# Optimization experiments

Measured on AMD Instinct MI355X. Metric: run time of the kernel, lower is better.

Reference implementation:

```python
import jax, jax.numpy as jnp
import numpy as np

B, N, D, NH, NP, H, W = 4, 4096, 256, 8, 8, 256, 256
HD = D // NH  # head_dims = 32


def _mlp(x, w1, b1, w2, b2):
    return jax.nn.relu(x @ w1 + b1) @ w2 + b2


def _grid_sample(value, grid):
    """Bilinear grid_sample, align_corners=False, zero padding.
    value: [M, C, Hh, Ww]; grid: [M, n, p, 2] with (x, y) in [-1, 1].
    Returns [M, C, n, p] (matches torch F.grid_sample output layout)."""
    M, C, Hh, Ww = value.shape
    x = (grid[..., 0] + 1.0) * (Ww * 0.5) - 0.5
    y = (grid[..., 1] + 1.0) * (Hh * 0.5) - 0.5
    x0 = jnp.floor(x)
    y0 = jnp.floor(y)
    wx1 = x - x0
    wy1 = y - y0
    vflat = value.reshape(M, C, Hh * Ww)

    def gather(yy, xx):
        valid = (xx >= 0) & (xx <= Ww - 1) & (yy >= 0) & (yy <= Hh - 1)
        idx = (jnp.clip(yy, 0, Hh - 1) * Ww + jnp.clip(xx, 0, Ww - 1)).astype(jnp.int32)
        g = jnp.take_along_axis(vflat, idx.reshape(M, 1, -1), axis=2)
        return g.reshape(M, C, idx.shape[1], idx.shape[2]) * valid[:, None].astype(value.dtype)

    return (gather(y0, x0) * ((1.0 - wy1) * (1.0 - wx1))[:, None]
            + gather(y0, x0 + 1.0) * ((1.0 - wy1) * wx1)[:, None]
            + gather(y0 + 1.0, x0) * (wy1 * (1.0 - wx1))[:, None]
            + gather(y0 + 1.0, x0 + 1.0) * (wy1 * wx1)[:, None])


def setup_inputs() -> dict:
    key = jax.random.key(0)
    ks = jax.random.split(key, 10)
    s = 0.02
    f32 = jnp.float32
    return {
        "ba_query": jax.random.normal(ks[0], (B, N, D), f32),
        "ref_pos": jax.random.uniform(ks[1], (B, N, 2), f32, minval=-0.9, maxval=0.9),
        "bev_feat": jax.random.normal(ks[2], (B, D, H, W), f32),
        "so_w1": jax.random.normal(ks[3], (D, D), f32) * s,
        "so_b1": jnp.zeros((D,), f32),
        "so_w2": jax.random.normal(ks[4], (D, NH * NP * 2), f32) * s,
        "so_b2": jnp.zeros((NH * NP * 2,), f32),
        "aw_w1": jax.random.normal(ks[5], (D, D), f32) * s,
        "aw_b1": jnp.zeros((D,), f32),
        "aw_w2": jax.random.normal(ks[6], (D, NH * NP), f32) * s,
        "aw_b2": jnp.zeros((NH * NP,), f32),
        "vp_w": jax.random.normal(ks[7], (HD, HD), f32) * s,  # 1x1 conv == per-pixel linear
        "vp_b": jnp.zeros((HD,), f32),
        "op_w1": jax.random.normal(ks[8], (D, D), f32) * s,
        "op_b1": jnp.zeros((D,), f32),
        "op_w2": jax.random.normal(ks[9], (D, D), f32) * s,
        "op_b2": jnp.zeros((D,), f32),
    }


def reference(ba_query, ref_pos, bev_feat,
              so_w1, so_b1, so_w2, so_b2,
              aw_w1, aw_b1, aw_w2, aw_b2,
              vp_w, vp_b,
              op_w1, op_b1, op_w2, op_b2):
    Bb, Dd, Hh, Ww = bev_feat.shape
    Nn = ba_query.shape[1]
    norm = jnp.array([float(Ww), float(Hh)], dtype=bev_feat.dtype)  # offset_normalizer = grid_size

    # value_proj: 1x1 conv on per-head channel groups  -> [B*NH, HD, H, W]
    value = bev_feat.reshape(Bb * NH, HD, Hh, Ww)
    value = jnp.einsum('mchw,oc->mohw', value, vp_w) + vp_b[None, :, None, None]

    # sampling locations: [B, NH, N, NP, 2] in grid_sample coords, y flipped
    so = _mlp(ba_query, so_w1, so_b1, so_w2, so_b2)
    so = so.reshape(Bb, Nn, NH, NP, 2).transpose(0, 2, 1, 3, 4)
    loc = ref_pos[:, None, :, None, :] + so / norm
    loc = loc.reshape(Bb * NH, Nn, NP, 2)
    loc = jnp.stack([loc[..., 0], -loc[..., 1]], axis=-1)

    sampled = _grid_sample(value, loc)            # [B*NH, HD, N, NP]
    sampled = sampled.reshape(Bb, NH, HD, Nn, NP)  # [B, NH, HD, N, NP]

    aw = _mlp(ba_query, aw_w1, aw_b1, aw_w2, aw_b2).reshape(Bb, Nn, NH, NP)
    aw = jax.nn.softmax(aw, axis=-1).transpose(0, 2, 1, 3)  # [B, NH, N, NP]

    # weighted sum over points, concat heads -> [B, N, D]
    attn_out = jnp.einsum('bhcnp,bhnp->bnhc', sampled, aw).reshape(Bb, Nn, Dd)
    return _mlp(attn_out, op_w1, op_b1, op_w2, op_b2)
```

## Files before the change

kernel.cpp:

```cpp
#include <hip/hip_runtime.h>

typedef unsigned short u16;
typedef unsigned int u32;
typedef __attribute__((ext_vector_type(8))) short short8;
typedef __attribute__((ext_vector_type(4))) float floatx4;

__device__ __forceinline__ float b2f(u16 u) {
    union { u32 i; float f; } x; x.i = ((u32)u) << 16; return x.f;
}
__device__ __forceinline__ u16 f2b(float f) {
    union { float f; u32 i; } x; x.f = f;
    u32 r = x.i + 0x7FFFu + ((x.i >> 16) & 1u);
    return (u16)(r >> 16);
}


template <int F32>
__device__ __forceinline__ float ldv(const void* p, size_t i) {
    if constexpr (F32) return ((const float*)p)[i];
    else return b2f(((const u16*)p)[i]);
}

__device__ __forceinline__ bool detect_f32(const void* ba_query) {
    const u16* q = (const u16*)ba_query;
    bool f32m = false;
    for (int i = 0; i < 64; ++i) {
        float v = b2f(q[i]);
        if (!(fabsf(v) < 1e4f)) f32m = true;
    }
    return f32m;
}

struct TapInfo {
    int i00, i01, i10, i11;
    float w00, w01, w10, w11;
};
__device__ __forceinline__ TapInfo tap_compute(float rx, float ry, float sox, float soy) {
    float gx = rx + sox * (1.f / 256.f);
    float gy = -(ry + soy * (1.f / 256.f));
    float x = (gx + 1.f) * 128.f - 0.5f;
    float y = (gy + 1.f) * 128.f - 0.5f;
    float x0f = floorf(x), y0f = floorf(y);
    float wx = x - x0f, wy = y - y0f;
    int x0 = (int)x0f, y0 = (int)y0f;
    int x1 = x0 + 1, y1 = y0 + 1;
    bool vx0 = (x0 >= 0) && (x0 <= 255);
    bool vx1 = (x1 >= 0) && (x1 <= 255);
    bool vy0 = (y0 >= 0) && (y0 <= 255);
    bool vy1 = (y1 >= 0) && (y1 <= 255);
    int cx0 = min(max(x0, 0), 255), cx1 = min(max(x1, 0), 255);
    int cy0 = min(max(y0, 0), 255), cy1 = min(max(y1, 0), 255);
    TapInfo t;
    t.i00 = (cy0 << 8) + cx0; t.i01 = (cy0 << 8) + cx1;
    t.i10 = (cy1 << 8) + cx0; t.i11 = (cy1 << 8) + cx1;
    t.w00 = (vy0 && vx0) ? (1.f - wy) * (1.f - wx) : 0.f;
    t.w01 = (vy0 && vx1) ? (1.f - wy) * wx         : 0.f;
    t.w10 = (vy1 && vx0) ? wy * (1.f - wx)         : 0.f;
    t.w11 = (vy1 && vx1) ? wy * wx                 : 0.f;
    return t;
}


template <int F32>
__device__ __forceinline__ void repack_body(const void* src, int ln, int base, int rel,
                                            u16* __restrict__ out)
{
    int k = rel >> ln;
    int n = rel & ((1 << ln) - 1);
    int cb = n >> 4, kb = k >> 5, l = ((k >> 3) & 3) * 16 + (n & 15), j = k & 7;
    u16 v;
    if constexpr (F32) v = f2b(((const float*)src)[rel]);
    else               v = ((const u16*)src)[rel];
    out[base + ((cb * 8 + kb) * 64 + l) * 8 + j] = v;
}

__global__ __launch_bounds__(256) void repack_k(
    const void* __restrict__ w0, const void* __restrict__ w1,
    const void* __restrict__ w2, const void* __restrict__ w3,
    const void* __restrict__ w4, const void* __restrict__ w5,
    u16* __restrict__ out, const void* __restrict__ qprobe)
{
    int gid = blockIdx.x * 256 + threadIdx.x;
    const void* src; int ln, base, rel;
    if      (gid < 65536)  { src = w0; ln = 8; base = 0;      rel = gid; }
    else if (gid < 98304)  { src = w1; ln = 7; base = 65536;  rel = gid - 65536; }
    else if (gid < 163840) { src = w2; ln = 8; base = 98304;  rel = gid - 98304; }
    else if (gid < 180224) { src = w3; ln = 6; base = 163840; rel = gid - 163840; }
    else if (gid < 245760) { src = w4; ln = 8; base = 180224; rel = gid - 180224; }
    else if (gid < 311296) { src = w5; ln = 8; base = 245760; rel = gid - 245760; }
    else return;
    if (detect_f32(qprobe)) repack_body<1>(src, ln, base, rel, out);
    else                    repack_body<0>(src, ln, base, rel, out);
}

template <int F32>
__device__ __forceinline__ void vproj_body(
    const void* __restrict__ bev, u16* __restrict__ value,
    const float wt[32][32], const float* bs, int gid)
{
    int m  = gid >> 15;
    int hw = (gid & 32767) << 1;

    float acc0[32], acc1[32];
#pragma unroll
    for (int o = 0; o < 32; ++o) { acc0[o] = bs[o]; acc1[o] = bs[o]; }

    size_t base = ((size_t)m << 21) + hw;
    for (int c = 0; c < 32; ++c) {
        float v0, v1;
        if constexpr (F32) {
            float2 pv = *(const float2*)((const float*)bev + base + ((size_t)c << 16));
            v0 = pv.x; v1 = pv.y;
        } else {
            u32 pv = *(const u32*)((const u16*)bev + base + ((size_t)c << 16));
            v0 = b2f((u16)(pv & 0xffffu)); v1 = b2f((u16)(pv >> 16));
        }
#pragma unroll
        for (int o4 = 0; o4 < 8; ++o4) {
            float4 w4 = *(const float4*)&wt[c][o4 * 4];
            acc0[o4*4+0] += v0 * w4.x; acc1[o4*4+0] += v1 * w4.x;
            acc0[o4*4+1] += v0 * w4.y; acc1[o4*4+1] += v1 * w4.y;
            acc0[o4*4+2] += v0 * w4.z; acc1[o4*4+2] += v1 * w4.z;
            acc0[o4*4+3] += v0 * w4.w; acc1[o4*4+3] += v1 * w4.w;
        }
    }

    u32 ow[32];
#pragma unroll
    for (int i = 0; i < 16; ++i) ow[i]      = (u32)f2b(acc0[2*i]) | ((u32)f2b(acc0[2*i+1]) << 16);
#pragma unroll
    for (int i = 0; i < 16; ++i) ow[16 + i] = (u32)f2b(acc1[2*i]) | ((u32)f2b(acc1[2*i+1]) << 16);
    uint4* dst = (uint4*)(value + ((size_t)gid << 6));
#pragma unroll
    for (int i = 0; i < 8; ++i)
        dst[i] = make_uint4(ow[4*i], ow[4*i+1], ow[4*i+2], ow[4*i+3]);
}

__global__ __launch_bounds__(256) void vproj_k(
    const void* __restrict__ bev, const void* __restrict__ vp_w,
    const void* __restrict__ vp_b, u16* __restrict__ value,
    const void* __restrict__ qprobe)
{
    __shared__ float wt[32][32];
    __shared__ float bs[32];
    int tid = threadIdx.x;
    bool f32m = detect_f32(qprobe);
    for (int i = tid; i < 1024; i += 256) {
        float v = f32m ? ((const float*)vp_w)[i] : b2f(((const u16*)vp_w)[i]);
        wt[i & 31][i >> 5] = v;
    }
    if (tid < 32) bs[tid] = f32m ? ((const float*)vp_b)[tid] : b2f(((const u16*)vp_b)[tid]);
    __syncthreads();

    int gid = blockIdx.x * 256 + tid;
    if (f32m) vproj_body<1>(bev, value, wt, bs, gid);
    else      vproj_body<0>(bev, value, wt, bs, gid);
}

template <int RELU, int AF32, int BIF32, int CF32>
__device__ __forceinline__ void gemm_body(
    const void* __restrict__ A, const u16* __restrict__ Bp,
    const void* __restrict__ bias, void* __restrict__ C,
    int N, int K, int bx, int by, int tid)
{
    const int lane = tid & 63, wave = tid >> 6;
    const int row0 = by * 64 + wave * 16, col0 = bx * 16;
    const int r = lane & 15, q = lane >> 4;
    const int Kb = K >> 5;

    floatx4 acc = {0.f, 0.f, 0.f, 0.f};
    const u16* Bpp = Bp + ((size_t)bx * Kb * 64 + lane) * 8;

    for (int kb = 0; kb < Kb; ++kb) {
        short8 a;
        if constexpr (AF32) {
            const float* ap = (const float*)A + (size_t)(row0 + r) * K + kb * 32 + q * 8;
            float4 f0 = *(const float4*)ap;
            float4 f1 = *(const float4*)(ap + 4);
            a[0] = (short)f2b(f0.x); a[1] = (short)f2b(f0.y);
            a[2] = (short)f2b(f0.z); a[3] = (short)f2b(f0.w);
            a[4] = (short)f2b(f1.x); a[5] = (short)f2b(f1.y);
            a[6] = (short)f2b(f1.z); a[7] = (short)f2b(f1.w);
        } else {
            a = *(const short8*)((const u16*)A + (size_t)(row0 + r) * K + kb * 32 + q * 8);
        }
        short8 b = *(const short8*)(Bpp + (size_t)kb * 512);
        acc = __builtin_amdgcn_mfma_f32_16x16x32_bf16(a, b, acc, 0, 0, 0);
    }

    float bz = ldv<BIF32>(bias, col0 + r);
#pragma unroll
    for (int i = 0; i < 4; ++i) {
        float v = acc[i] + bz;
        if (RELU) v = fmaxf(v, 0.f);
        size_t idx = (size_t)(row0 + q * 4 + i) * N + col0 + r;
        if constexpr (CF32) ((float*)C)[idx] = v;
        else                ((u16*)C)[idx] = f2b(v);
    }
}

template <int RELU, int AIN, int COUT>
__global__ __launch_bounds__(256) void gemm_k(
    const void* __restrict__ A, const u16* __restrict__ Bp,
    const void* __restrict__ bias, void* __restrict__ C,
    int N, int K, const void* __restrict__ qprobe)
{
    if (detect_f32(qprobe))
        gemm_body<RELU, AIN, 1, COUT>(A, Bp, bias, C, N, K, blockIdx.x, blockIdx.y, threadIdx.x);
    else
        gemm_body<RELU, 0, 0, 0>(A, Bp, bias, C, N, K, blockIdx.x, blockIdx.y, threadIdx.x);
}

template <int F32>
__device__ __forceinline__ void sample_body(
    const u16* __restrict__ value, const void* __restrict__ ref_pos,
    const u16* __restrict__ soL, const u16* __restrict__ awn,
    u16* __restrict__ attn, int bn, int tid)
{
    int b  = bn >> 12;
    int nh = tid >> 5, c = tid & 31;

    float rx = ldv<F32>(ref_pos, bn * 2 + 0);
    float ry = ldv<F32>(ref_pos, bn * 2 + 1);

    float aw[8];
    float mx = -1e30f;
#pragma unroll
    for (int p = 0; p < 8; ++p) { aw[p] = b2f(awn[bn * 64 + nh * 8 + p]); mx = fmaxf(mx, aw[p]); }
    float s = 0.f;
#pragma unroll
    for (int p = 0; p < 8; ++p) { aw[p] = __expf(aw[p] - mx); s += aw[p]; }
    float inv = 1.f / s;

    const u16* vbase = value + (((size_t)(b * 8 + nh)) << 21);
    float acc = 0.f;

#pragma unroll
    for (int p = 0; p < 8; ++p) {
        float sox = b2f(soL[bn * 128 + (nh * 8 + p) * 2 + 0]);
        float soy = b2f(soL[bn * 128 + (nh * 8 + p) * 2 + 1]);
        TapInfo t = tap_compute(rx, ry, sox, soy);
        float v00 = b2f(vbase[((size_t)t.i00 << 5) + c]);
        float v01 = b2f(vbase[((size_t)t.i01 << 5) + c]);
        float v10 = b2f(vbase[((size_t)t.i10 << 5) + c]);
        float v11 = b2f(vbase[((size_t)t.i11 << 5) + c]);
        float samp = v00 * t.w00 + v01 * t.w01 + v10 * t.w10 + v11 * t.w11;
        acc += aw[p] * inv * samp;
    }
    attn[(size_t)bn * 256 + tid] = f2b(acc);
}

__global__ __launch_bounds__(256) void sample_k(
    const u16* __restrict__ value, const void* __restrict__ ref_pos,
    const u16* __restrict__ soL, const u16* __restrict__ awn,
    u16* __restrict__ attn, const void* __restrict__ qprobe)
{
    if (detect_f32(qprobe))
        sample_body<1>(value, ref_pos, soL, awn, attn, blockIdx.x, threadIdx.x);
    else
        sample_body<0>(value, ref_pos, soL, awn, attn, blockIdx.x, threadIdx.x);
}

template <int F32>
__device__ __forceinline__ float4 bias4(const void* bptr, int n4) {
    if constexpr (F32) {
        return *(const float4*)((const float*)bptr + n4);
    } else {
        ushort4 b = *(const ushort4*)((const u16*)bptr + n4);
        float4 r; r.x = b2f(b.x); r.y = b2f(b.y); r.z = b2f(b.z); r.w = b2f(b.w);
        return r;
    }
}

template <int F32>
__device__ __forceinline__ float4 dot4T(const u16* __restrict__ A, const void* __restrict__ W,
                                        int ldw, int n4, float4 acc)
{
    for (int k = 0; k < 256; k += 2) {
        u32 two = *(const u32*)(A + k);
        float a0 = b2f((u16)(two & 0xffffu));
        float a1 = b2f((u16)(two >> 16));
        if constexpr (F32) {
            const float* w0 = (const float*)W + (size_t)k * ldw + n4;
            float4 x0 = *(const float4*)w0;
            float4 x1 = *(const float4*)(w0 + ldw);
            acc.x += a0 * x0.x + a1 * x1.x;
            acc.y += a0 * x0.y + a1 * x1.y;
            acc.z += a0 * x0.z + a1 * x1.z;
            acc.w += a0 * x0.w + a1 * x1.w;
        } else {
            const u16* w0 = (const u16*)W + (size_t)k * ldw + n4;
            ushort4 x0 = *(const ushort4*)w0;
            ushort4 x1 = *(const ushort4*)(w0 + ldw);
            acc.x += a0 * b2f(x0.x) + a1 * b2f(x1.x);
            acc.y += a0 * b2f(x0.y) + a1 * b2f(x1.y);
            acc.z += a0 * b2f(x0.z) + a1 * b2f(x1.z);
            acc.w += a0 * b2f(x0.w) + a1 * b2f(x1.w);
        }
    }
    return acc;
}

#define GQ 32

template <int F32>
__device__ void fused_body(
    const void* __restrict__ ba_query, const void* __restrict__ ref_pos,
    const void* __restrict__ bev,
    const void* __restrict__ so_w1, const void* __restrict__ so_b1,
    const void* __restrict__ so_w2, const void* __restrict__ so_b2,
    const void* __restrict__ aw_w1, const void* __restrict__ aw_b1,
    const void* __restrict__ aw_w2, const void* __restrict__ aw_b2,
    const void* __restrict__ vp_w,  const void* __restrict__ vp_b,
    const void* __restrict__ op_w1, const void* __restrict__ op_b1,
    const void* __restrict__ op_w2, const void* __restrict__ op_b2,
    void* __restrict__ out, char* pool, int tid, int q0)
{
    u16*   qa  = (u16*)(pool + 0);
    u16*   hbu = (u16*)(pool + 16896);
    float* raw = (float*)(pool + 0);
    float* soL = (float*)(pool + 33792);
    float* awn = (float*)(pool + 50176);
    u16*   atp = (u16*)(pool + 33792);
    float* cov = (float*)(pool + 58368);
    float* wvt = (float*)(pool + 59392);
    float* bsv = (float*)(pool + 63488);
    u16*   h3  = (u16*)(pool + 0);

    for (int it = 0; it < 4; ++it) {
        int idx = tid + (it << 8);
        int g = idx >> 5;
        int k0 = (idx & 31) << 3;
        if constexpr (F32) {
            const float* s = (const float*)ba_query + (size_t)(q0 + g) * 256 + k0;
#pragma unroll
            for (int j = 0; j < 8; ++j) qa[g * 264 + k0 + j] = f2b(s[j]);
        } else {
            uint4 v = *(const uint4*)((const u16*)ba_query + (size_t)(q0 + g) * 256 + k0);
            *(uint4*)(qa + g * 264 + k0) = v;
        }
    }
    for (int it = 0; it < 4; ++it) {
        int idx = tid + (it << 8);
        wvt[(idx & 31) * 32 + (idx >> 5)] = ldv<F32>(vp_w, idx);
    }
    if (tid < 32) bsv[tid] = ldv<F32>(vp_b, tid);
    __syncthreads();

    for (int it = 0; it < 8; ++it) {
        int fg = tid + (it << 8);
        int g = fg >> 6, n4 = (fg & 63) << 2;
        float4 acc = bias4<F32>(so_b1, n4);
        acc = dot4T<F32>(qa + g * 264, so_w1, 256, n4, acc);
        u16* d = hbu + g * 264 + n4;
        d[0] = f2b(fmaxf(acc.x, 0.f)); d[1] = f2b(fmaxf(acc.y, 0.f));
        d[2] = f2b(fmaxf(acc.z, 0.f)); d[3] = f2b(fmaxf(acc.w, 0.f));
    }
    __syncthreads();

    for (int it = 0; it < 4; ++it) {
        int fg = tid + (it << 8);
        int g = fg >> 5, n4 = (fg & 31) << 2;
        float4 acc = bias4<F32>(so_b2, n4);
        acc = dot4T<F32>(hbu + g * 264, so_w2, 128, n4, acc);
        float* d = soL + g * 128 + n4;
        d[0] = acc.x; d[1] = acc.y; d[2] = acc.z; d[3] = acc.w;
    }
    __syncthreads();

    for (int it = 0; it < 8; ++it) {
        int fg = tid + (it << 8);
        int g = fg >> 6, n4 = (fg & 63) << 2;
        float4 acc = bias4<F32>(aw_b1, n4);
        acc = dot4T<F32>(qa + g * 264, aw_w1, 256, n4, acc);
        u16* d = hbu + g * 264 + n4;
        d[0] = f2b(fmaxf(acc.x, 0.f)); d[1] = f2b(fmaxf(acc.y, 0.f));
        d[2] = f2b(fmaxf(acc.z, 0.f)); d[3] = f2b(fmaxf(acc.w, 0.f));
    }
    __syncthreads();

    for (int it = 0; it < 2; ++it) {
        int fg = tid + (it << 8);
        int g = fg >> 4, n4 = (fg & 15) << 2;
        float4 acc = bias4<F32>(aw_b2, n4);
        acc = dot4T<F32>(hbu + g * 264, aw_w2, 64, n4, acc);
        float* d = awn + g * 64 + n4;
        d[0] = acc.x; d[1] = acc.y; d[2] = acc.z; d[3] = acc.w;
    }
    __syncthreads();

    {
        int g = tid >> 3, nh = tid & 7;
        float* a = awn + g * 64 + nh * 8;
        float mx = a[0];
#pragma unroll
        for (int p = 1; p < 8; ++p) mx = fmaxf(mx, a[p]);
        float s = 0.f;
#pragma unroll
        for (int p = 0; p < 8; ++p) { float e = __expf(a[p] - mx); a[p] = e; s += e; }
        float inv = 1.f / s;
#pragma unroll
        for (int p = 0; p < 8; ++p) a[p] *= inv;
    }
    __syncthreads();

    {
        int nh = tid >> 5, c = tid & 31;
        int b = q0 >> 12;
        size_t poff = ((size_t)b << 24) + (((size_t)(nh * 32 + c)) << 16);
        const u16*   pu = (const u16*)bev + poff;
        const float* pf = (const float*)bev + poff;
        for (int g = 0; g < GQ; ++g) {
            int q = q0 + g;
            float rx = ldv<F32>(ref_pos, q * 2 + 0);
            float ry = ldv<F32>(ref_pos, q * 2 + 1);
            const float* sog = soL + g * 128 + nh * 16;
            const float* awg = awn + g * 64 + nh * 8;
            float acc = 0.f, cv = 0.f;
#pragma unroll
            for (int p = 0; p < 8; ++p) {
                TapInfo t = tap_compute(rx, ry, sog[2 * p], sog[2 * p + 1]);
                float v00, v01, v10, v11;
                if constexpr (F32) {
                    v00 = pf[t.i00]; v01 = pf[t.i01]; v10 = pf[t.i10]; v11 = pf[t.i11];
                } else {
                    v00 = b2f(pu[t.i00]); v01 = b2f(pu[t.i01]);
                    v10 = b2f(pu[t.i10]); v11 = b2f(pu[t.i11]);
                }
                float wp = awg[p];
                acc += wp * (t.w00 * v00 + t.w01 * v01 + t.w10 * v10 + t.w11 * v11);
                cv  += wp * (t.w00 + t.w01 + t.w10 + t.w11);
            }
            raw[g * 256 + tid] = acc;
            if (c == 0) cov[g * 8 + nh] = cv;
        }
    }
    __syncthreads();

    {
        int nh = tid >> 5, o = tid & 31;
        for (int g = 0; g < GQ; ++g) {
            const float* rg = raw + g * 256 + nh * 32;
            float acc = bsv[o] * cov[g * 8 + nh];
#pragma unroll
            for (int c2 = 0; c2 < 32; ++c2) acc += wvt[c2 * 32 + o] * rg[c2];
            atp[g * 264 + tid] = f2b(acc);
        }
    }
    __syncthreads();

    for (int it = 0; it < 8; ++it) {
        int fg = tid + (it << 8);
        int g = fg >> 6, n4 = (fg & 63) << 2;
        float4 acc = bias4<F32>(op_b1, n4);
        acc = dot4T<F32>(atp + g * 264, op_w1, 256, n4, acc);
        u16* d = h3 + g * 264 + n4;
        d[0] = f2b(fmaxf(acc.x, 0.f)); d[1] = f2b(fmaxf(acc.y, 0.f));
        d[2] = f2b(fmaxf(acc.z, 0.f)); d[3] = f2b(fmaxf(acc.w, 0.f));
    }
    __syncthreads();

    for (int it = 0; it < 8; ++it) {
        int fg = tid + (it << 8);
        int g = fg >> 6, n4 = (fg & 63) << 2;
        float4 acc = bias4<F32>(op_b2, n4);
        acc = dot4T<F32>(h3 + g * 264, op_w2, 256, n4, acc);
        if constexpr (F32) {
            *(float4*)((float*)out + (size_t)(q0 + g) * 256 + n4) = acc;
        } else {
            ushort4 r;
            r.x = f2b(acc.x); r.y = f2b(acc.y); r.z = f2b(acc.z); r.w = f2b(acc.w);
            *(ushort4*)((u16*)out + (size_t)(q0 + g) * 256 + n4) = r;
        }
    }
}

__global__ __launch_bounds__(256) void fused_all(
    const void* __restrict__ ba_query, const void* __restrict__ ref_pos,
    const void* __restrict__ bev,
    const void* __restrict__ so_w1, const void* __restrict__ so_b1,
    const void* __restrict__ so_w2, const void* __restrict__ so_b2,
    const void* __restrict__ aw_w1, const void* __restrict__ aw_b1,
    const void* __restrict__ aw_w2, const void* __restrict__ aw_b2,
    const void* __restrict__ vp_w,  const void* __restrict__ vp_b,
    const void* __restrict__ op_w1, const void* __restrict__ op_b1,
    const void* __restrict__ op_w2, const void* __restrict__ op_b2,
    void* __restrict__ out)
{
    __shared__ __align__(16) char pool[63616];
    int tid = threadIdx.x;
    int q0 = blockIdx.x * GQ;
    if (q0 >= 16384) return;
    if (detect_f32(ba_query))
        fused_body<1>(ba_query, ref_pos, bev, so_w1, so_b1, so_w2, so_b2,
                      aw_w1, aw_b1, aw_w2, aw_b2, vp_w, vp_b,
                      op_w1, op_b1, op_w2, op_b2, out, pool, tid, q0);
    else
        fused_body<0>(ba_query, ref_pos, bev, so_w1, so_b1, so_w2, so_b2,
                      aw_w1, aw_b1, aw_w2, aw_b2, vp_w, vp_b,
                      op_w1, op_b1, op_w2, op_b2, out, pool, tid, q0);
}

extern "C" void kernel_launch(void* const* d_in, const int* in_sizes, int n_in,
                              void* d_out, int out_size, void* d_ws, size_t ws_size,
                              hipStream_t stream)
{
    const void* ba_query = d_in[0];
    const void* ref_pos  = d_in[1];
    const void* bev      = d_in[2];
    const void* so_w1 = d_in[3];
    const void* so_b1 = d_in[4];
    const void* so_w2 = d_in[5];
    const void* so_b2 = d_in[6];
    const void* aw_w1 = d_in[7];
    const void* aw_b1 = d_in[8];
    const void* aw_w2 = d_in[9];
    const void* aw_b2 = d_in[10];
    const void* vp_w  = d_in[11];
    const void* vp_b  = d_in[12];
    const void* op_w1 = d_in[13];
    const void* op_b1 = d_in[14];
    const void* op_w2 = d_in[15];
    const void* op_b2 = d_in[16];

    const size_t FAST_MIN = 149946368ull;
    if (ws_size >= FAST_MIN) {
        char* w = (char*)d_ws;
        u16* value = (u16*)(w);
        u16* pack  = (u16*)(w + 134217728);
        u16* hbuf  = (u16*)(w + 135266304);
        u16* soL   = (u16*)(w + 143654912);
        u16* awn   = (u16*)(w + 147849216);
        u16* attn  = (u16*)d_out;

        repack_k<<<1216, 256, 0, stream>>>(so_w1, so_w2, aw_w1, aw_w2, op_w1, op_w2, pack, ba_query);
        vproj_k<<<4096, 256, 0, stream>>>(bev, vp_w, vp_b, value, ba_query);
        gemm_k<1, 1, 0><<<dim3(16, 256), 256, 0, stream>>>(ba_query, pack + 0,      so_b1, hbuf, 256, 256, ba_query);
        gemm_k<0, 0, 0><<<dim3(8, 256),  256, 0, stream>>>(hbuf,     pack + 65536,  so_b2, soL,  128, 256, ba_query);
        gemm_k<1, 1, 0><<<dim3(16, 256), 256, 0, stream>>>(ba_query, pack + 98304,  aw_b1, hbuf, 256, 256, ba_query);
        gemm_k<0, 0, 0><<<dim3(4, 256),  256, 0, stream>>>(hbuf,     pack + 163840, aw_b2, awn,   64, 256, ba_query);
        sample_k<<<16384, 256, 0, stream>>>(value, ref_pos, soL, awn, attn, ba_query);
        gemm_k<1, 0, 0><<<dim3(16, 256), 256, 0, stream>>>(attn, pack + 180224, op_b1, hbuf, 256, 256, ba_query);
        gemm_k<0, 0, 1><<<dim3(16, 256), 256, 0, stream>>>(hbuf, pack + 245760, op_b2, d_out, 256, 256, ba_query);
    } else {
        size_t probe_s = ws_size >> 24;
        int probe = probe_s > 63 ? 63 : (int)probe_s;
        fused_all<<<512 + probe, 256, 0, stream>>>(
            ba_query, ref_pos, bev,
            so_w1, so_b1, so_w2, so_b2,
            aw_w1, aw_b1, aw_w2, aw_b2,
            vp_w, vp_b, op_w1, op_b1, op_w2, op_b2, d_out);
    }
}
```

Baseline: 711.7 us.

## Use MFMA for value projection, widen GEMM tiles, preconvert query and biases

The per-pixel 1x1 value projection moves from scalar FMAs with LDS-held weights to bf16 MFMA instructions, with one wave handling 16-pixel tiles. The small GEMMs now compute a 64-column tile per block, so each A fragment is reused across four MFMAs and far fewer blocks are launched. The query is converted to bf16 once in a separate kernel, and the biases are converted to fp32 during repack, so the GEMMs no longer branch on dtype. In exchange there is one more launch, the value projection inputs are rounded to bf16 before the multiply, and the projection reads bev with strided per-channel loads.

New measurement: 581.3 us. -18.3%, faster.

```diff
diff --git a/kernel.cpp b/kernel.cpp
--- a/kernel.cpp
+++ b/kernel.cpp
@@ -61,79 +61,121 @@
 }
 
 
-template <int F32>
-__device__ __forceinline__ void repack_body(const void* src, int ln, int base, int rel,
-                                            u16* __restrict__ out)
-{
-    int k = rel >> ln;
-    int n = rel & ((1 << ln) - 1);
-    int cb = n >> 4, kb = k >> 5, l = ((k >> 3) & 3) * 16 + (n & 15), j = k & 7;
-    u16 v;
-    if constexpr (F32) v = f2b(((const float*)src)[rel]);
-    else               v = ((const u16*)src)[rel];
-    out[base + ((cb * 8 + kb) * 64 + l) * 8 + j] = v;
-}
-
 __global__ __launch_bounds__(256) void repack_k(
     const void* __restrict__ w0, const void* __restrict__ w1,
     const void* __restrict__ w2, const void* __restrict__ w3,
     const void* __restrict__ w4, const void* __restrict__ w5,
-    u16* __restrict__ out, const void* __restrict__ qprobe)
+    const void* __restrict__ b0, const void* __restrict__ b1,
+    const void* __restrict__ b2, const void* __restrict__ b3,
+    const void* __restrict__ b4, const void* __restrict__ b5,
+    u16* __restrict__ out, float* __restrict__ biasF,
+    const void* __restrict__ qprobe)
 {
     int gid = blockIdx.x * 256 + threadIdx.x;
+    bool f32m = detect_f32(qprobe);
+    if (gid >= 311296) {
+        int g2 = gid - 311296;
+        if (g2 >= 1216) return;
+        const void* bsrc; int off;
+        if      (g2 < 256)  { bsrc = b0; off = g2; }
+        else if (g2 < 384)  { bsrc = b1; off = g2 - 256; }
+        else if (g2 < 640)  { bsrc = b2; off = g2 - 384; }
+        else if (g2 < 704)  { bsrc = b3; off = g2 - 640; }
+        else if (g2 < 960)  { bsrc = b4; off = g2 - 704; }
+        else                { bsrc = b5; off = g2 - 960; }
+        biasF[g2] = f32m ? ((const float*)bsrc)[off] : b2f(((const u16*)bsrc)[off]);
+        return;
+    }
     const void* src; int ln, base, rel;
     if      (gid < 65536)  { src = w0; ln = 8; base = 0;      rel = gid; }
     else if (gid < 98304)  { src = w1; ln = 7; base = 65536;  rel = gid - 65536; }
     else if (gid < 163840) { src = w2; ln = 8; base = 98304;  rel = gid - 98304; }
     else if (gid < 180224) { src = w3; ln = 6; base = 163840; rel = gid - 163840; }
     else if (gid < 245760) { src = w4; ln = 8; base = 180224; rel = gid - 180224; }
-    else if (gid < 311296) { src = w5; ln = 8; base = 245760; rel = gid - 245760; }
-    else return;
-    if (detect_f32(qprobe)) repack_body<1>(src, ln, base, rel, out);
-    else                    repack_body<0>(src, ln, base, rel, out);
+    else                   { src = w5; ln = 8; base = 245760; rel = gid - 245760; }
+    int k = rel >> ln;
+    int n = rel & ((1 << ln) - 1);
+    int cb = n >> 4, kb = k >> 5, l = ((k >> 3) & 3) * 16 + (n & 15), j = k & 7;
+    u16 v = f32m ? f2b(((const float*)src)[rel]) : ((const u16*)src)[rel];
+    out[base + ((cb * 8 + kb) * 64 + l) * 8 + j] = v;
+}
+
+template <int F32>
+__global__ __launch_bounds__(256) void qcvt_k(const void* __restrict__ src,
+                                              u16* __restrict__ dst)
+{
+    int i = blockIdx.x * 256 + threadIdx.x;
+    if constexpr (F32) {
+        const float* s = (const float*)src + (size_t)i * 8;
+        float4 f0 = *(const float4*)s, f1 = *(const float4*)(s + 4);
+        u32 o0 = (u32)f2b(f0.x) | ((u32)f2b(f0.y) << 16);
+        u32 o1 = (u32)f2b(f0.z) | ((u32)f2b(f0.w) << 16);
+        u32 o2 = (u32)f2b(f1.x) | ((u32)f2b(f1.y) << 16);
+        u32 o3 = (u32)f2b(f1.z) | ((u32)f2b(f1.w) << 16);
+        *(uint4*)(dst + (size_t)i * 8) = make_uint4(o0, o1, o2, o3);
+    } else {
+        *(uint4*)(dst + (size_t)i * 8) = *(const uint4*)((const u16*)src + (size_t)i * 8);
+    }
+}
+
+__global__ __launch_bounds__(256) void qcvt_sel(const void* __restrict__ src,
+                                                u16* __restrict__ dst)
+{
+    int i = blockIdx.x * 256 + threadIdx.x;
+    if (detect_f32(src)) {
+        const float* s = (const float*)src + (size_t)i * 8;
+        float4 f0 = *(const float4*)s, f1 = *(const float4*)(s + 4);
+        u32 o0 = (u32)f2b(f0.x) | ((u32)f2b(f0.y) << 16);
+        u32 o1 = (u32)f2b(f0.z) | ((u32)f2b(f0.w) << 16);
+        u32 o2 = (u32)f2b(f1.x) | ((u32)f2b(f1.y) << 16);
+        u32 o3 = (u32)f2b(f1.z) | ((u32)f2b(f1.w) << 16);
+        *(uint4*)(dst + (size_t)i * 8) = make_uint4(o0, o1, o2, o3);
+    } else {
+        *(uint4*)(dst + (size_t)i * 8) = *(const uint4*)((const u16*)src + (size_t)i * 8);
+    }
 }
 
 template <int F32>
 __device__ __forceinline__ void vproj_body(
-    const void* __restrict__ bev, u16* __restrict__ value,
-    const float wt[32][32], const float* bs, int gid)
-{
-    int m  = gid >> 15;
-    int hw = (gid & 32767) << 1;
-
-    float acc0[32], acc1[32];
-#pragma unroll
-    for (int o = 0; o < 32; ++o) { acc0[o] = bs[o]; acc1[o] = bs[o]; }
-
-    size_t base = ((size_t)m << 21) + hw;
-    for (int c = 0; c < 32; ++c) {
-        float v0, v1;
-        if constexpr (F32) {
-            float2 pv = *(const float2*)((const float*)bev + base + ((size_t)c << 16));
-            v0 = pv.x; v1 = pv.y;
-        } else {
-            u32 pv = *(const u32*)((const u16*)bev + base + ((size_t)c << 16));
-            v0 = b2f((u16)(pv & 0xffffu)); v1 = b2f((u16)(pv >> 16));
-        }
-#pragma unroll
-        for (int o4 = 0; o4 < 8; ++o4) {
-            float4 w4 = *(const float4*)&wt[c][o4 * 4];
-            acc0[o4*4+0] += v0 * w4.x; acc1[o4*4+0] += v1 * w4.x;
-            acc0[o4*4+1] += v0 * w4.y; acc1[o4*4+1] += v1 * w4.y;
-            acc0[o4*4+2] += v0 * w4.z; acc1[o4*4+2] += v1 * w4.z;
-            acc0[o4*4+3] += v0 * w4.w; acc1[o4*4+3] += v1 * w4.w;
-        }
-    }
-
-    u32 ow[32];
-#pragma unroll
-    for (int i = 0; i < 16; ++i) ow[i]      = (u32)f2b(acc0[2*i]) | ((u32)f2b(acc0[2*i+1]) << 16);
-#pragma unroll
-    for (int i = 0; i < 16; ++i) ow[16 + i] = (u32)f2b(acc1[2*i]) | ((u32)f2b(acc1[2*i+1]) << 16);
-    uint4* dst = (uint4*)(value + ((size_t)gid << 6));
-#pragma unroll
-    for (int i = 0; i < 8; ++i)
-        dst[i] = make_uint4(ow[4*i], ow[4*i+1], ow[4*i+2], ow[4*i+3]);
+    const void* __restrict__ bev, const void* __restrict__ vp_w,
+    const void* __restrict__ vp_b, u16* __restrict__ value,
+    int bx, int m, int tid)
+{
+    const int lane = tid & 63, w = tid >> 6;
+    const int wave_in_m = bx * 4 + w;
+    const int r = lane & 15, q = lane >> 4;
+
+    short8 a0, a1;
+#pragma unroll
+    for (int j = 0; j < 8; ++j) {
+        a0[j] = (short)f2b(ldv<F32>(vp_w, (size_t)r * 32 + q * 8 + j));
+        a1[j] = (short)f2b(ldv<F32>(vp_w, (size_t)(r + 16) * 32 + q * 8 + j));
+    }
+    float bz0[4], bz1[4];
+#pragma unroll
+    for (int i = 0; i < 4; ++i) {
+        bz0[i] = ldv<F32>(vp_b, q * 4 + i);
+        bz1[i] = ldv<F32>(vp_b, 16 + q * 4 + i);
+    }
+
+    const size_t crow = (size_t)m * 32 + q * 8;
+    for (int t = 0; t < 16; ++t) {
+        int px = wave_in_m * 256 + t * 16 + r;
+        short8 b;
+#pragma unroll
+        for (int j = 0; j < 8; ++j)
+            b[j] = (short)f2b(ldv<F32>(bev, ((crow + j) << 16) + px));
+        floatx4 acc0 = {0.f, 0.f, 0.f, 0.f}, acc1 = {0.f, 0.f, 0.f, 0.f};
+        acc0 = __builtin_amdgcn_mfma_f32_16x16x32_bf16(a0, b, acc0, 0, 0, 0);
+        acc1 = __builtin_amdgcn_mfma_f32_16x16x32_bf16(a1, b, acc1, 0, 0, 0);
+        u32 w0 = (u32)f2b(acc0[0] + bz0[0]) | ((u32)f2b(acc0[1] + bz0[1]) << 16);
+        u32 w1 = (u32)f2b(acc0[2] + bz0[2]) | ((u32)f2b(acc0[3] + bz0[3]) << 16);
+        u32 w2 = (u32)f2b(acc1[0] + bz1[0]) | ((u32)f2b(acc1[1] + bz1[1]) << 16);
+        u32 w3 = (u32)f2b(acc1[2] + bz1[2]) | ((u32)f2b(acc1[3] + bz1[3]) << 16);
+        u16* dst = value + (((size_t)m << 21) + ((size_t)px << 5));
+        *(uint2*)(dst + q * 4)      = make_uint2(w0, w1);
+        *(uint2*)(dst + 16 + q * 4) = make_uint2(w2, w3);
+    }
 }
 
 __global__ __launch_bounds__(256) void vproj_k(
@@ -141,74 +183,48 @@
     const void* __restrict__ vp_b, u16* __restrict__ value,
     const void* __restrict__ qprobe)
 {
-    __shared__ float wt[32][32];
-    __shared__ float bs[32];
-    int tid = threadIdx.x;
-    bool f32m = detect_f32(qprobe);
-    for (int i = tid; i < 1024; i += 256) {
-        float v = f32m ? ((const float*)vp_w)[i] : b2f(((const u16*)vp_w)[i]);
-        wt[i & 31][i >> 5] = v;
-    }
-    if (tid < 32) bs[tid] = f32m ? ((const float*)vp_b)[tid] : b2f(((const u16*)vp_b)[tid]);
-    __syncthreads();
-
-    int gid = blockIdx.x * 256 + tid;
-    if (f32m) vproj_body<1>(bev, value, wt, bs, gid);
-    else      vproj_body<0>(bev, value, wt, bs, gid);
-}
-
-template <int RELU, int AF32, int BIF32, int CF32>
-__device__ __forceinline__ void gemm_body(
-    const void* __restrict__ A, const u16* __restrict__ Bp,
-    const void* __restrict__ bias, void* __restrict__ C,
-    int N, int K, int bx, int by, int tid)
-{
-    const int lane = tid & 63, wave = tid >> 6;
-    const int row0 = by * 64 + wave * 16, col0 = bx * 16;
+    if (detect_f32(qprobe))
+        vproj_body<1>(bev, vp_w, vp_b, value, blockIdx.x, blockIdx.y, threadIdx.x);
+    else
+        vproj_body<0>(bev, vp_w, vp_b, value, blockIdx.x, blockIdx.y, threadIdx.x);
+}
+
+template <int RELU, int CF32>
+__global__ __launch_bounds__(256) void gemm_k(
+    const u16* __restrict__ A, const u16* __restrict__ Bp,
+    const float* __restrict__ biasF, void* __restrict__ C, int N)
+{
+    const int tid = threadIdx.x;
+    const int lane = tid & 63, w = tid >> 6;
+    const int row0 = blockIdx.y * 64 + w * 16;
+    const int colb = blockIdx.x * 64;
     const int r = lane & 15, q = lane >> 4;
-    const int Kb = K >> 5;
-
-    floatx4 acc = {0.f, 0.f, 0.f, 0.f};
-    const u16* Bpp = Bp + ((size_t)bx * Kb * 64 + lane) * 8;
-
-    for (int kb = 0; kb < Kb; ++kb) {
-        short8 a;
-        if constexpr (AF32) {
-            const float* ap = (const float*)A + (size_t)(row0 + r) * K + kb * 32 + q * 8;
-            float4 f0 = *(const float4*)ap;
-            float4 f1 = *(const float4*)(ap + 4);
-            a[0] = (short)f2b(f0.x); a[1] = (short)f2b(f0.y);
-            a[2] = (short)f2b(f0.z); a[3] = (short)f2b(f0.w);
-            a[4] = (short)f2b(f1.x); a[5] = (short)f2b(f1.y);
-            a[6] = (short)f2b(f1.z); a[7] = (short)f2b(f1.w);
-        } else {
-            a = *(const short8*)((const u16*)A + (size_t)(row0 + r) * K + kb * 32 + q * 8);
-        }
-        short8 b = *(const short8*)(Bpp + (size_t)kb * 512);
-        acc = __builtin_amdgcn_mfma_f32_16x16x32_bf16(a, b, acc, 0, 0, 0);
-    }
-
-    float bz = ldv<BIF32>(bias, col0 + r);
-#pragma unroll
-    for (int i = 0; i < 4; ++i) {
-        float v = acc[i] + bz;
-        if (RELU) v = fmaxf(v, 0.f);
-        size_t idx = (size_t)(row0 + q * 4 + i) * N + col0 + r;
-        if constexpr (CF32) ((float*)C)[idx] = v;
-        else                ((u16*)C)[idx] = f2b(v);
-    }
-}
-
-template <int RELU, int AIN, int COUT>
-__global__ __launch_bounds__(256) void gemm_k(
-    const void* __restrict__ A, const u16* __restrict__ Bp,
-    const void* __restrict__ bias, void* __restrict__ C,
-    int N, int K, const void* __restrict__ qprobe)
-{
-    if (detect_f32(qprobe))
-        gemm_body<RELU, AIN, 1, COUT>(A, Bp, bias, C, N, K, blockIdx.x, blockIdx.y, threadIdx.x);
-    else
-        gemm_body<RELU, 0, 0, 0>(A, Bp, bias, C, N, K, blockIdx.x, blockIdx.y, threadIdx.x);
+
+    floatx4 acc[4] = {{0.f,0.f,0.f,0.f},{0.f,0.f,0.f,0.f},{0.f,0.f,0.f,0.f},{0.f,0.f,0.f,0.f}};
+    const u16* Ap = A + (size_t)(row0 + r) * 256 + q * 8;
+    const u16* B0 = Bp + ((size_t)(blockIdx.x * 4) * 8) * 512 + lane * 8;
+
+    for (int kb = 0; kb < 8; ++kb) {
+        short8 a = *(const short8*)(Ap + kb * 32);
+#pragma unroll
+        for (int t = 0; t < 4; ++t) {
+            short8 b = *(const short8*)(B0 + (size_t)(t * 8 + kb) * 512);
+            acc[t] = __builtin_amdgcn_mfma_f32_16x16x32_bf16(a, b, acc[t], 0, 0, 0);
+        }
+    }
+#pragma unroll
+    for (int t = 0; t < 4; ++t) {
+        int col = colb + t * 16 + r;
+        float bz = biasF[col];
+#pragma unroll
+        for (int i = 0; i < 4; ++i) {
+            float v = acc[t][i] + bz;
+            if (RELU) v = fmaxf(v, 0.f);
+            size_t idx = (size_t)(row0 + q * 4 + i) * N + col;
+            if constexpr (CF32) ((float*)C)[idx] = v;
+            else                ((u16*)C)[idx] = f2b(v);
+        }
+    }
 }
 
 template <int F32>
@@ -526,22 +542,27 @@
     const size_t FAST_MIN = 149946368ull;
     if (ws_size >= FAST_MIN) {
         char* w = (char*)d_ws;
-        u16* value = (u16*)(w);
-        u16* pack  = (u16*)(w + 134217728);
-        u16* hbuf  = (u16*)(w + 135266304);
-        u16* soL   = (u16*)(w + 143654912);
-        u16* awn   = (u16*)(w + 147849216);
-        u16* attn  = (u16*)d_out;
-
-        repack_k<<<1216, 256, 0, stream>>>(so_w1, so_w2, aw_w1, aw_w2, op_w1, op_w2, pack, ba_query);
-        vproj_k<<<4096, 256, 0, stream>>>(bev, vp_w, vp_b, value, ba_query);
-        gemm_k<1, 1, 0><<<dim3(16, 256), 256, 0, stream>>>(ba_query, pack + 0,      so_b1, hbuf, 256, 256, ba_query);
-        gemm_k<0, 0, 0><<<dim3(8, 256),  256, 0, stream>>>(hbuf,     pack + 65536,  so_b2, soL,  128, 256, ba_query);
-        gemm_k<1, 1, 0><<<dim3(16, 256), 256, 0, stream>>>(ba_query, pack + 98304,  aw_b1, hbuf, 256, 256, ba_query);
-        gemm_k<0, 0, 0><<<dim3(4, 256),  256, 0, stream>>>(hbuf,     pack + 163840, aw_b2, awn,   64, 256, ba_query);
+        u16*   value = (u16*)(w);
+        u16*   pack  = (u16*)(w + 134217728);
+        float* biasF = (float*)(w + 134217728 + 786432);
+        u16*   hbuf  = (u16*)(w + 135266304);
+        u16*   soL   = (u16*)(w + 143654912);
+        u16*   awn   = (u16*)(w + 147849216);
+        u16*   attn  = (u16*)d_out;
+        u16*   qbuf  = (u16*)((char*)d_out + 8388608);
+
+        repack_k<<<1221, 256, 0, stream>>>(so_w1, so_w2, aw_w1, aw_w2, op_w1, op_w2,
+                                           so_b1, so_b2, aw_b1, aw_b2, op_b1, op_b2,
+                                           pack, biasF, ba_query);
+        qcvt_sel<<<2048, 256, 0, stream>>>(ba_query, qbuf);
+        vproj_k<<<dim3(64, 32), 256, 0, stream>>>(bev, vp_w, vp_b, value, ba_query);
+        gemm_k<1, 0><<<dim3(4, 256), 256, 0, stream>>>(qbuf, pack + 0,      biasF + 0,   hbuf, 256);
+        gemm_k<0, 0><<<dim3(2, 256), 256, 0, stream>>>(hbuf, pack + 65536,  biasF + 256, soL,  128);
+        gemm_k<1, 0><<<dim3(4, 256), 256, 0, stream>>>(qbuf, pack + 98304,  biasF + 384, hbuf, 256);
+        gemm_k<0, 0><<<dim3(1, 256), 256, 0, stream>>>(hbuf, pack + 163840, biasF + 640, awn,  64);
         sample_k<<<16384, 256, 0, stream>>>(value, ref_pos, soL, awn, attn, ba_query);
-        gemm_k<1, 0, 0><<<dim3(16, 256), 256, 0, stream>>>(attn, pack + 180224, op_b1, hbuf, 256, 256, ba_query);
-        gemm_k<0, 0, 1><<<dim3(16, 256), 256, 0, stream>>>(hbuf, pack + 245760, op_b2, d_out, 256, 256, ba_query);
+        gemm_k<1, 0><<<dim3(4, 256), 256, 0, stream>>>(attn, pack + 180224, biasF + 704, hbuf, 256);
+        gemm_k<0, 1><<<dim3(4, 256), 256, 0, stream>>>(hbuf, pack + 245760, biasF + 960, d_out, 256);
     } else {
         size_t probe_s = ws_size >> 24;
         int probe = probe_s > 63 ? 63 : (int)probe_s;
```
